# Optimization experiments

Measured on AMD Instinct MI355X. Metric: run time of the kernel, lower is better.

Reference implementation:

```python
import jax, jax.numpy as jnp
import numpy as np

B, T, D, N, K, H = 2, 2048, 2048, 16, 8, 128
WIN = 1024                      # sliding_window_size
SOFT_CAP = 50.0                 # attn_logits_soft_cap
SCALAR = 0.08838834764831845    # query_pre_attn_scalar = head_dim**-0.5
K_MASK = -2.3819763e+38
ROPE_BASE = 10000.0
ROPE_SCALE = 1.0


def apply_rope(x, positions):
    # x: [B, T, heads, H]; positions: [B, T]
    head_dim = x.shape[-1]
    half = head_dim // 2
    timescale = ROPE_BASE ** (2.0 * jnp.arange(half, dtype=jnp.float32) / head_dim)
    sinusoid = positions[..., None].astype(jnp.float32) / timescale / ROPE_SCALE  # [B,T,half]
    sin = jnp.sin(sinusoid)[:, :, None, :]
    cos = jnp.cos(sinusoid)[:, :, None, :]
    first, second = jnp.split(x, 2, axis=-1)
    return jnp.concatenate(
        [first * cos - second * sin, second * cos + first * sin], axis=-1
    ).astype(x.dtype)


def setup_inputs() -> dict:
    key = jax.random.key(0)
    k0, k1, k2, k3 = jax.random.split(key, 4)
    x = jax.random.normal(k0, (B, T, D), jnp.float32)
    wq = jax.random.normal(k1, (N, D, H), jnp.float32) * (D ** -0.5)
    wkv = jax.random.normal(k2, (2, K, D, H), jnp.float32) * (D ** -0.5)
    wo = jax.random.normal(k3, (N, H, D), jnp.float32) * ((N * H) ** -0.5)
    segment_pos = jnp.broadcast_to(jnp.arange(T, dtype=jnp.int32), (B, T))
    attn_mask = jnp.broadcast_to(jnp.tril(jnp.ones((T, T), dtype=bool)), (B, T, T))  # causal
    return {"x": x, "wq": wq, "wkv": wkv, "wo": wo,
            "segment_pos": segment_pos, "attn_mask": attn_mask}


def reference(x, wq, wkv, wo, segment_pos, attn_mask):
    # --- projections ---
    q = jnp.einsum('BTD,NDH->BTNH', x, wq)          # [B,T,N,H]
    kv = jnp.einsum('BTD,CKDH->CBTKH', x, wkv)      # [2,B,T,K,H]
    k_proj, v_proj = kv[0], kv[1]
    # --- RoPE + query scaling ---
    q = apply_rope(q, segment_pos) * SCALAR
    k_proj = apply_rope(k_proj, segment_pos)
    # --- GQA logits ---
    G = N // K
    qg = q.reshape(B, T, K, G, H)
    logits = jnp.einsum('BTKGH,BSKH->BTKGS', qg, k_proj).reshape(B, T, N, T)
    # --- soft cap ---
    logits = jnp.tanh(logits / SOFT_CAP) * SOFT_CAP
    # --- sliding-window mask combined with causal attn_mask ---
    all_ones = jnp.ones(attn_mask.shape, dtype=attn_mask.dtype)
    sliding_mask = jnp.triu(all_ones, -WIN + 1) * jnp.tril(all_ones, WIN - 1)
    mask = sliding_mask * attn_mask                  # [B,T,S]
    padded_logits = jnp.where(mask[:, :, None, :], logits, K_MASK)
    probs = jax.nn.softmax(padded_logits, axis=-1).astype(k_proj.dtype)
    # --- GQA weighted values ---
    encoded = jnp.einsum('BTKGS,BSKH->BTKGH',
                         probs.reshape(B, T, K, G, T), v_proj).reshape(B, T, N, H)
    # --- output projection ---
    return jnp.einsum('BTNH,NHD->BTD', encoded, wo)
```

## Files before the change

### kernel.cpp

```cpp
#include <hip/hip_runtime.h>
#include <stdint.h>

#define BDIM 2
#define TDIM 2048
#define DDIM 2048
#define NHEADS 16
#define KVH 8
#define HDIM 128
#define WINSZ 1024
#define BT (BDIM*TDIM)
#define NHD (NHEADS*HDIM)
#define QKVC 4096

typedef unsigned short u16;
typedef __attribute__((ext_vector_type(8))) short bf16x8;
typedef __attribute__((ext_vector_type(4))) float f32x4;

__device__ __forceinline__ u16 f2bf(float f) {
  union { float f; unsigned u; } v; v.f = f;
  unsigned r = v.u + 0x7FFFu + ((v.u >> 16) & 1u);
  return (u16)(r >> 16);
}
__device__ __forceinline__ float bf2f(u16 u) {
  union { unsigned u; float f; } v; v.u = ((unsigned)u) << 16;
  return v.f;
}

__device__ __forceinline__ void gl_lds16(const u16* g, u16* l) {
  __builtin_amdgcn_global_load_lds((const __attribute__((address_space(1))) void*)g,
                                   (__attribute__((address_space(3))) void*)l, 16, 0, 0);
}

__global__ __launch_bounds__(256) void k_prep(const float* __restrict__ x, const float* __restrict__ wq,
                                              const float* __restrict__ wkv, const float* __restrict__ wo,
                                              const int* __restrict__ seg,
                                              u16* __restrict__ x_bf, u16* __restrict__ wt_qkv,
                                              u16* __restrict__ wo_t, float2* __restrict__ tab) {
  const int id = blockIdx.x, tid = threadIdx.x;
  if (id < 8192) {
    __shared__ float tl0[32][33];
    int tx = tid & 31, ty = tid >> 5;
    int r0 = (id & 127) * 32, c0 = (id >> 7) * 32;
    #pragma unroll
    for (int i = 0; i < 4; i++) {
      int r = r0 + tx, c = c0 + ty + i*8;
      const float* sp; size_t off;
      if (r < 2048) { sp = wq; off = (size_t)(r >> 7)*262144u + (size_t)(r & 127); }
      else { int j = r - 2048; sp = wkv; off = (size_t)((j >> 10)*8 + ((j >> 7) & 7))*262144u + (size_t)(j & 127); }
      off += (size_t)c * 128u;
      tl0[tx][ty + i*8] = sp[off];
    }
    __syncthreads();
    #pragma unroll
    for (int i = 0; i < 4; i++) {
      int rl = ty + i*8;
      wt_qkv[(size_t)(r0 + rl)*2048u + (size_t)(c0 + tx)] = f2bf(tl0[rl][tx]);
    }
  } else if (id < 16384) {
    int i = (id - 8192)*256 + tid;
    float4 v = ((const float4*)x)[i];
    ushort4 o;
    o.x = f2bf(v.x); o.y = f2bf(v.y); o.z = f2bf(v.z); o.w = f2bf(v.w);
    ((ushort4*)x_bf)[i] = o;
  } else if (id < 20480) {
    __shared__ float tl1[32][33];
    int id3 = id - 16384;
    int tx = tid & 31, ty = tid >> 5;
    int r0 = (id3 & 63) * 32, c0 = (id3 >> 6) * 32;
    #pragma unroll
    for (int i = 0; i < 4; i++) {
      int r = r0 + tx, c = c0 + ty + i*8;
      tl1[tx][ty + i*8] = wo[(size_t)c * 2048u + (size_t)r];
    }
    __syncthreads();
    #pragma unroll
    for (int i = 0; i < 4; i++) {
      int rl = ty + i*8;
      wo_t[(size_t)(r0 + rl)*2048u + (size_t)(c0 + tx)] = f2bf(tl1[rl][tx]);
    }
  } else {
    int bt = (id - 20480)*4 + (tid >> 6);
    int i = tid & 63;
    int pos = seg[bt];
    float inv_ts = exp2f(-(float)i * (13.287712379549449f/64.0f));
    float ang = (float)pos * inv_ts;
    tab[(size_t)bt*64 + i] = make_float2(cosf(ang), sinf(ang));
  }
}

template<int F32OUT>
__global__ __launch_bounds__(256) void k_gemm(const u16* __restrict__ A, const u16* __restrict__ Bt,
                                              void* __restrict__ Cout, int M, int Ncols, int Kdim, int ldc) {
  __shared__ u16 As[128*64];
  __shared__ u16 Bs[128*64];
  const int tid = threadIdx.x, lane = tid & 63, wave = tid >> 6;
  const int bid = blockIdx.x;
  const int xcd = bid & 7, idx = bid >> 3;
  const int m0 = (((xcd & 3) << 3) + (idx & 7)) * 128;
  const int n0 = (((xcd >> 2) << 3) + (idx >> 3)) * 128;
  const int wr = wave >> 1, wc = wave & 1;
  const int l15 = lane & 15, lg = lane >> 4;
  f32x4 acc[4][4] = {};
  for (int kt = 0; kt < Kdim; kt += 64) {
    __syncthreads();
    #pragma unroll
    for (int i = 0; i < 4; i++) {
      int chb = i*256 + wave*64;
      int ch = chb + lane;
      int r = ch >> 3, cc = ch & 7;
      gl_lds16(A + (size_t)(m0 + r)*Kdim + kt + cc*8, As + chb*8);
      gl_lds16(Bt + (size_t)(n0 + r)*Kdim + kt + cc*8, Bs + chb*8);
    }
    __syncthreads();
    #pragma unroll
    for (int ks = 0; ks < 2; ks++) {
      bf16x8 af[4], bf[4];
      int kk = ks*32 + lg*8;
      #pragma unroll
      for (int mt = 0; mt < 4; mt++) af[mt] = *(const bf16x8*)(As + (wr*64 + mt*16 + l15)*64 + kk);
      #pragma unroll
      for (int nt = 0; nt < 4; nt++) bf[nt] = *(const bf16x8*)(Bs + (wc*64 + nt*16 + l15)*64 + kk);
      #pragma unroll
      for (int mt = 0; mt < 4; mt++)
        #pragma unroll
        for (int nt = 0; nt < 4; nt++)
          acc[mt][nt] = __builtin_amdgcn_mfma_f32_16x16x32_bf16(af[mt], bf[nt], acc[mt][nt], 0, 0, 0);
    }
  }
  #pragma unroll
  for (int mt = 0; mt < 4; mt++) {
    int row = m0 + wr*64 + mt*16 + lg*4;
    #pragma unroll
    for (int nt = 0; nt < 4; nt++) {
      int col = n0 + wc*64 + nt*16 + l15;
      #pragma unroll
      for (int j = 0; j < 4; j++) {
        if (F32OUT) ((float*)Cout)[(size_t)(row + j)*ldc + col] = acc[mt][nt][j];
        else        ((u16*)Cout)[(size_t)(row + j)*ldc + col] = f2bf(acc[mt][nt][j]);
      }
    }
  }
}

template<int F32OUT>
__global__ __launch_bounds__(512, 2) void k_gemm8(const u16* __restrict__ A, const u16* __restrict__ Bt,
                                                  void* __restrict__ Cout, int M, int Ncols, int Kdim, int ldc) {
  __shared__ u16 As[2][256*64];
  __shared__ u16 Bs[2][256*64];
  const int tid = threadIdx.x, lane = tid & 63, wave = tid >> 6;
  const int l15 = lane & 15, lg = lane >> 4;
  const int wm = wave >> 2, wn = wave & 3;
  const int gx = M >> 8, gy = Ncols >> 8;
  const int nwg = gx * gy;
  int bid = blockIdx.x;
  int q = nwg >> 3, r = nwg & 7;
  int xcd = bid & 7, idx = bid >> 3;
  int wg = (xcd < r ? xcd*(q+1) : r*(q+1) + (xcd - r)*q) + idx;
  const int m0 = (wg % gx) * 256, n0 = (wg / gx) * 256;

  const int st_r = tid >> 3;
  const int st_c = (tid & 7) ^ (st_r & 7);

  const u16* Ag = A + (size_t)(m0 + st_r)*Kdim + st_c*8;
  const u16* Bg = Bt + (size_t)(n0 + st_r)*Kdim + st_c*8;

  auto stage = [&](int t, int h) {
    int buf = t & 1;
    if (h < 2) {
      const u16* g = Bg + (size_t)(h*128)*Kdim + t*64;
      u16* d = &Bs[buf][h*8192 + wave*512];
      gl_lds16(g, d);
      gl_lds16(g + (size_t)64*Kdim, d + 4096);
    } else {
      int hh = h - 2;
      const u16* g = Ag + (size_t)(hh*128)*Kdim + t*64;
      u16* d = &As[buf][hh*8192 + wave*512];
      gl_lds16(g, d);
      gl_lds16(g + (size_t)64*Kdim, d + 4096);
    }
  };

  const int aBase = (wm*128 + l15) * 128;
  const int bBase = (wn*64 + l15) * 128;
  const int kx0 = ((lg) ^ (l15 & 7)) << 4;
  const int kx1 = ((4 + lg) ^ (l15 & 7)) << 4;

  f32x4 acc[8][4] = {};
  bf16x8 af[4][2], bfr[4][2];

  stage(0,0); stage(0,1); stage(0,2); stage(0,3);
  asm volatile("s_waitcnt vmcnt(4)" ::: "memory");
  stage(1,0); stage(1,1); stage(1,2);
  asm volatile("s_waitcnt vmcnt(6)" ::: "memory");
  __builtin_amdgcn_s_barrier();

  const int NT = Kdim >> 6;

#define MFMA_Q(MS, NS)                                                          \
  { _Pragma("unroll") for (int mf = 0; mf < 4; mf++)                            \
    _Pragma("unroll") for (int nf = 0; nf < 2; nf++) {                          \
      acc[(MS)+mf][(NS)+nf] = __builtin_amdgcn_mfma_f32_16x16x32_bf16(af[mf][0], bfr[(NS)+nf][0], acc[(MS)+mf][(NS)+nf], 0, 0, 0); \
      acc[(MS)+mf][(NS)+nf] = __builtin_amdgcn_mfma_f32_16x16x32_bf16(af[mf][1], bfr[(NS)+nf][1], acc[(MS)+mf][(NS)+nf], 0, 0, 0); \
  } }

  for (int t = 0; t < NT; ++t) {
    const int cur = t & 1;
    const char* Ab = (const char*)&As[cur][0];
    const char* Bb = (const char*)&Bs[cur][0];
    #pragma unroll
    for (int mf = 0; mf < 4; mf++) {
      af[mf][0] = *(const bf16x8*)(Ab + aBase + mf*2048 + kx0);
      af[mf][1] = *(const bf16x8*)(Ab + aBase + mf*2048 + kx1);
    }
    #pragma unroll
    for (int nf = 0; nf < 2; nf++) {
      bfr[nf][0] = *(const bf16x8*)(Bb + bBase + nf*2048 + kx0);
      bfr[nf][1] = *(const bf16x8*)(Bb + bBase + nf*2048 + kx1);
    }
    if (t + 1 < NT) stage(t+1, 3);
    asm volatile("s_waitcnt lgkmcnt(8)" ::: "memory");
    __builtin_amdgcn_s_barrier();
    asm volatile("" ::: "memory");
    __builtin_amdgcn_s_setprio(1);
    MFMA_Q(0, 0)
    __builtin_amdgcn_s_setprio(0);
    __builtin_amdgcn_s_barrier();
    #pragma unroll
    for (int nf = 2; nf < 4; nf++) {
      bfr[nf][0] = *(const bf16x8*)(Bb + bBase + nf*2048 + kx0);
      bfr[nf][1] = *(const bf16x8*)(Bb + bBase + nf*2048 + kx1);
    }
    __builtin_amdgcn_s_barrier();
    asm volatile("" ::: "memory");
    __builtin_amdgcn_s_setprio(1);
    MFMA_Q(0, 2)
    __builtin_amdgcn_s_setprio(0);
    __builtin_amdgcn_s_barrier();
    #pragma unroll
    for (int mf = 0; mf < 4; mf++) {
      af[mf][0] = *(const bf16x8*)(Ab + aBase + 8192 + mf*2048 + kx0);
      af[mf][1] = *(const bf16x8*)(Ab + aBase + 8192 + mf*2048 + kx1);
    }
    if (t + 2 < NT) { stage(t+2, 0); stage(t+2, 1); }
    __builtin_amdgcn_s_barrier();
    asm volatile("" ::: "memory");
    __builtin_amdgcn_s_setprio(1);
    MFMA_Q(4, 2)
    __builtin_amdgcn_s_setprio(0);
    __builtin_amdgcn_s_barrier();
    if (t + 2 < NT) {
      stage(t+2, 2);
      asm volatile("s_waitcnt vmcnt(6)" ::: "memory");
    } else if (t + 1 < NT) {
      asm volatile("s_waitcnt vmcnt(0)" ::: "memory");
    }
    __builtin_amdgcn_s_barrier();
    asm volatile("" ::: "memory");
    __builtin_amdgcn_s_setprio(1);
    MFMA_Q(4, 0)
    __builtin_amdgcn_s_setprio(0);
    __builtin_amdgcn_s_barrier();
  }
#undef MFMA_Q

  #pragma unroll
  for (int mf = 0; mf < 8; mf++) {
    int row = m0 + wm*128 + mf*16 + lg*4;
    #pragma unroll
    for (int nf = 0; nf < 4; nf++) {
      int col = n0 + wn*64 + nf*16 + l15;
      #pragma unroll
      for (int j = 0; j < 4; j++) {
        if (F32OUT) ((float*)Cout)[(size_t)(row + j)*ldc + col] = acc[mf][nf][j];
        else        ((u16*)Cout)[(size_t)(row + j)*ldc + col] = f2bf(acc[mf][nf][j]);
      }
    }
  }
}

__global__ __launch_bounds__(256) void k_kvt(u16* __restrict__ qkv, const float2* __restrict__ tab,
                                             u16* __restrict__ vT) {
  const int id = blockIdx.x, tid = threadIdx.x;
  if (id < 4096) {
    const int bt = id;
    const int kh = tid >> 5, ii = (tid & 31) * 2;
    u16* row = qkv + (size_t)bt*QKVC + 2048 + kh*128 + ii;
    const float2 c0 = tab[(size_t)bt*64 + ii];
    const float2 c1 = tab[(size_t)bt*64 + ii + 1];
    unsigned fu = *(const unsigned*)row;
    unsigned su = *(const unsigned*)(row + 64);
    float f0 = bf2f((u16)(fu & 0xffff)), f1 = bf2f((u16)(fu >> 16));
    float s0 = bf2f((u16)(su & 0xffff)), s1 = bf2f((u16)(su >> 16));
    unsigned ro = (unsigned)f2bf(f0*c0.x - s0*c0.y) | ((unsigned)f2bf(f1*c1.x - s1*c1.y) << 16);
    unsigned rs = (unsigned)f2bf(s0*c0.x + f0*c0.y) | ((unsigned)f2bf(s1*c1.x + f1*c1.y) << 16);
    *(unsigned*)row = ro;
    *(unsigned*)(row + 64) = rs;
  } else {
    __shared__ u16 tl[32][33];
    const int id2 = id - 4096;
    const int tx = tid & 31, ty = tid >> 5;
    const int t0 = (id2 & 63)*32, h0 = ((id2 >> 6) & 3)*32, bk = id2 >> 8;
    const u16* src = qkv + (size_t)(bk >> 3)*TDIM*QKVC + 3072 + (bk & 7)*HDIM;
    #pragma unroll
    for (int i = 0; i < 4; i++)
      tl[ty + i*8][tx] = src[(size_t)(t0 + ty + i*8)*QKVC + h0 + tx];
    __syncthreads();
    u16* dst = vT + (size_t)bk*HDIM*TDIM;
    #pragma unroll
    for (int i = 0; i < 4; i++)
      dst[(size_t)(h0 + ty + i*8)*TDIM + t0 + tx] = tl[tx][ty + i*8];
  }
}

__device__ __forceinline__ void stage_tiles(const u16* __restrict__ kg, const u16* __restrict__ vg,
                                            u16* ldsK, u16* ldsV, int tid) {
  const int w = tid >> 6;
  const int rK = tid >> 4, cK = tid & 15;
  u16* dK = ldsK + w*512;
  gl_lds16(kg + (size_t)rK*QKVC + ((cK ^ (rK & 15)) << 3), dK);
  gl_lds16(kg + (size_t)(rK + 32)*QKVC + ((cK ^ ((rK + 32) & 15)) << 3), dK + 4096);
  const int rV = tid >> 3, cV = tid & 7;
  u16* dV = ldsV + w*512;
  gl_lds16(vg + (size_t)rV*TDIM + ((cV ^ (rV & 7)) << 3), dV);
  gl_lds16(vg + (size_t)(rV + 64)*TDIM + ((cV ^ ((rV + 64) & 7)) << 3), dV + 4096);
}

__global__ __launch_bounds__(512, 4) void k_attn(const u16* __restrict__ qkv, const u16* __restrict__ vT,
                                                 const float2* __restrict__ tab, u16* __restrict__ enc) {
  __shared__ u16 Kb[2][64*128];
  __shared__ u16 Vb[2][128*64];
  __shared__ u16 Pl[8][16*64];
  const int tid = threadIdx.x;
  const int lane = tid & 63, wave = tid >> 6;
  const int l15 = lane & 15, lg = lane >> 4;
  const int wg = blockIdx.x;
  const int lin = (wg & 7)*64 + (wg >> 3);
  const int qt = lin & 31, kvh = (lin >> 5) & 7, b = lin >> 8;
  const int n = kvh*2 + (wave >> 2);
  const int t0 = qt * 64;
  const int lo_row = t0 + (wave & 3)*16, hi_row = lo_row + 15;

  bf16x8 qf[4];
  {
    const int qrow = b*TDIM + lo_row + l15;
    const u16* qb = qkv + (size_t)qrow*QKVC + n*HDIM + lg*8;
    #pragma unroll
    for (int ks = 0; ks < 4; ks++) qf[ks] = *(const bf16x8*)(qb + ks*32);
    const float2* trow = tab + (size_t)qrow*64 + lg*8;
    const float SC = 0.08838834764831845f;
    #pragma unroll
    for (int ks = 0; ks < 2; ks++)
      #pragma unroll
      for (int e = 0; e < 8; e++) {
        float2 cs = trow[ks*32 + e];
        float f = bf2f((u16)qf[ks][e]), s = bf2f((u16)qf[ks+2][e]);
        qf[ks][e]   = (short)f2bf((f*cs.x - s*cs.y) * SC);
        qf[ks+2][e] = (short)f2bf((s*cs.x + f*cs.y) * SC);
      }
  }
  f32x4 o[8] = {};
  f32x4 o_l = {};
  const short one_bf = (short)0x3F80;
  const bf16x8 ones = {one_bf, one_bf, one_bf, one_bf, one_bf, one_bf, one_bf, one_bf};

  const u16* kgb = qkv + (size_t)(b*TDIM)*QKVC + 2048 + kvh*HDIM;
  const u16* vgb = vT + (size_t)(b*KVH + kvh)*HDIM*TDIM;

  const float L0 = 1.4426950408889634f;
  const float L1 = -1.9235933878519513e-4f;
  const float L2 = 3.0777094205631089e-8f;
  const float BIAS = -72.13475204444817f;

  const int s_begin = (t0 >= 1024) ? (t0 - 1024) : 0;
  stage_tiles(kgb + (size_t)s_begin*QKVC, vgb + s_begin, Kb[0], Vb[0], tid);
  int cur = 0;
  for (int s0 = s_begin; s0 <= t0; s0 += 64) {
    if (s0 + 64 <= t0) {
      stage_tiles(kgb + (size_t)(s0 + 64)*QKVC, vgb + (s0 + 64), Kb[cur ^ 1], Vb[cur ^ 1], tid);
      asm volatile("s_waitcnt vmcnt(4)" ::: "memory");
    } else {
      asm volatile("s_waitcnt vmcnt(0)" ::: "memory");
    }
    __builtin_amdgcn_s_barrier();
    __builtin_amdgcn_sched_barrier(0);

    const u16* Kc = Kb[cur];
    const u16* Vc = Vb[cur];
    f32x4 sc4[4];
    #pragma unroll
    for (int c = 0; c < 4; c++) {
      const int cLo = s0 + c*16;
      bool anyLive = (cLo <= hi_row) && (cLo + 15 >= lo_row - (WINSZ - 1));
      bool full    = (cLo + 15 <= lo_row) && (cLo >= hi_row - (WINSZ - 1));
      f32x4 a = {0.f, 0.f, 0.f, 0.f};
      if (anyLive) {
        int krow = c*16 + l15;
        __builtin_amdgcn_s_setprio(1);
        #pragma unroll
        for (int ks = 0; ks < 4; ks++) {
          bf16x8 kf = *(const bf16x8*)(Kc + krow*128 + (((ks*4 + lg) ^ l15) << 3));
          a = __builtin_amdgcn_mfma_f32_16x16x32_bf16(qf[ks], kf, a, 0, 0, 0);
        }
        __builtin_amdgcn_s_setprio(0);
        if (full) {
          #pragma unroll
          for (int j = 0; j < 4; j++) {
            float z = a[j];
            float u = z*z;
            float tt = __builtin_fmaf(u, __builtin_fmaf(u, L2, L1), L0);
            a[j] = exp2f(__builtin_fmaf(z, tt, BIAS));
          }
        } else {
          #pragma unroll
          for (int j = 0; j < 4; j++) {
            int scol = cLo + l15;
            int trow2 = lo_row + lg*4 + j;
            float z = a[j];
            float u = z*z;
            float tt = __builtin_fmaf(u, __builtin_fmaf(u, L2, L1), L0);
            float p = exp2f(__builtin_fmaf(z, tt, BIAS));
            bool ok = (scol <= trow2) && (scol >= trow2 - (WINSZ - 1));
            a[j] = ok ? p : 0.f;
          }
        }
      }
      sc4[c] = a;
    }
    #pragma unroll
    for (int c = 0; c < 4; c++)
      #pragma unroll
      for (int j = 0; j < 4; j++) {
        int prow = lg*4 + j, pcol = c*16 + l15;
        int off = prow*128 + pcol*2; off ^= (prow & 7) << 4;
        *(u16*)((char*)(&Pl[wave][0]) + off) = f2bf(sc4[c][j]);
      }
    __builtin_amdgcn_s_setprio(1);
    #pragma unroll
    for (int ks = 0; ks < 2; ks++) {
      int roff = l15*128 + ks*64 + lg*16; roff ^= (l15 & 7) << 4;
      bf16x8 pf = *(const bf16x8*)((char*)(&Pl[wave][0]) + roff);
      o_l = __builtin_amdgcn_mfma_f32_16x16x32_bf16(pf, ones, o_l, 0, 0, 0);
      #pragma unroll
      for (int ct = 0; ct < 8; ct++) {
        int vrow = ct*16 + l15;
        bf16x8 vf = *(const bf16x8*)(Vc + vrow*64 + (((ks*4 + lg) ^ (l15 & 7)) << 3));
        o[ct] = __builtin_amdgcn_mfma_f32_16x16x32_bf16(pf, vf, o[ct], 0, 0, 0);
      }
    }
    __builtin_amdgcn_s_setprio(0);
    __builtin_amdgcn_s_barrier();
    cur ^= 1;
  }
  #pragma unroll
  for (int j = 0; j < 4; j++) {
    float inv = __fdividef(1.f, o_l[j]);
    int row = lo_row + lg*4 + j;
    u16* eb = enc + (size_t)(b*TDIM + row)*NHD + n*HDIM;
    #pragma unroll
    for (int ct = 0; ct < 8; ct++)
      eb[ct*16 + l15] = f2bf(o[ct][j] * inv);
  }
}

extern "C" void kernel_launch(void* const* d_in, const int* in_sizes, int n_in,
                              void* d_out, int out_size, void* d_ws, size_t ws_size,
                              hipStream_t stream) {
  const float* x   = (const float*)d_in[0];
  const float* wq  = (const float*)d_in[1];
  const float* wkv = (const float*)d_in[2];
  const float* wo  = (const float*)d_in[3];
  const int*   seg = (const int*)d_in[4];
  float* out = (float*)d_out;

  char* ws = (char*)d_ws;
  u16*    x_bf   = (u16*)(ws);
  u16*    wt_qkv = (u16*)(ws + (16u << 20));
  u16*    qkv    = (u16*)(ws + (32u << 20));
  u16*    vT     = (u16*)(ws + (64u << 20));
  u16*    enc    = (u16*)(ws + (72u << 20));
  u16*    wo_t   = (u16*)(ws + (88u << 20));
  float2* tab    = (float2*)(ws + (96u << 20));

  k_prep<<<dim3(21504), 256, 0, stream>>>(x, wq, wkv, wo, seg, x_bf, wt_qkv, wo_t, tab);
  k_gemm8<0><<<dim3((BT/256)*(QKVC/256)), 512, 0, stream>>>(x_bf, wt_qkv, qkv, BT, QKVC, DDIM, QKVC);
  k_kvt<<<dim3(8192), 256, 0, stream>>>(qkv, tab, vT);
  k_attn<<<dim3(512), 512, 0, stream>>>(qkv, vT, tab, enc);
  k_gemm<1><<<dim3(512), 256, 0, stream>>>(enc, wo_t, out, BT, DDIM, NHD, DDIM);
}
```

Baseline: 207.0 us.

## Fuse RoPE and query scaling into QKV GEMM epilogue

Each wave in the QKV GEMM now owns column pairs 64 apart within a head, instead of a contiguous 64-column slab. This lets the epilogue apply RoPE to Q and K, plus the query scale, in registers before the bf16 store. The separate K-RoPE pass in the old kvt kernel is dropped, leaving a V-transpose-only kernel, and the per-block Q RoPE in the attention kernel is removed. The aim is to avoid extra global read/write passes over K and the redundant Q RoPE work in attention. The trade-offs are a strided B-fragment LDS read pattern, a table load in the GEMM epilogue, and bf16 conversion switched to the library intrinsic.

```diff
diff --git a/kernel.cpp b/kernel.cpp
--- a/kernel.cpp
+++ b/kernel.cpp
@@ -1,4 +1,5 @@
 #include <hip/hip_runtime.h>
+#include <hip/hip_bf16.h>
 #include <stdint.h>
 
 #define BDIM 2
@@ -24,6 +25,10 @@
 __device__ __forceinline__ float bf2f(u16 u) {
   union { unsigned u; float f; } v; v.u = ((unsigned)u) << 16;
   return v.f;
+}
+__device__ __forceinline__ u16 cvt_bf(float f) {
+  __hip_bfloat16 hb = __float2bfloat16(f);
+  return *reinterpret_cast<u16*>(&hb);
 }
 
 __device__ __forceinline__ void gl_lds16(const u16* g, u16* l) {
@@ -142,9 +147,9 @@
   }
 }
 
-template<int F32OUT>
 __global__ __launch_bounds__(512, 2) void k_gemm8(const u16* __restrict__ A, const u16* __restrict__ Bt,
-                                                  void* __restrict__ Cout, int M, int Ncols, int Kdim, int ldc) {
+                                                  u16* __restrict__ Cout, const float2* __restrict__ tab,
+                                                  int M, int Ncols, int Kdim, int ldc) {
   __shared__ u16 As[2][256*64];
   __shared__ u16 Bs[2][256*64];
   const int tid = threadIdx.x, lane = tid & 63, wave = tid >> 6;
@@ -181,7 +186,7 @@
   };
 
   const int aBase = (wm*128 + l15) * 128;
-  const int bBase = (wn*64 + l15) * 128;
+  const int bBase = (wn*16 + l15) * 128;
   const int kx0 = ((lg) ^ (l15 & 7)) << 4;
   const int kx1 = ((4 + lg) ^ (l15 & 7)) << 4;
 
@@ -214,8 +219,8 @@
     }
     #pragma unroll
     for (int nf = 0; nf < 2; nf++) {
-      bfr[nf][0] = *(const bf16x8*)(Bb + bBase + nf*2048 + kx0);
-      bfr[nf][1] = *(const bf16x8*)(Bb + bBase + nf*2048 + kx1);
+      bfr[nf][0] = *(const bf16x8*)(Bb + bBase + nf*8192 + kx0);
+      bfr[nf][1] = *(const bf16x8*)(Bb + bBase + nf*8192 + kx1);
     }
     if (t + 1 < NT) stage(t+1, 3);
     asm volatile("s_waitcnt lgkmcnt(8)" ::: "memory");
@@ -227,8 +232,8 @@
     __builtin_amdgcn_s_barrier();
     #pragma unroll
     for (int nf = 2; nf < 4; nf++) {
-      bfr[nf][0] = *(const bf16x8*)(Bb + bBase + nf*2048 + kx0);
-      bfr[nf][1] = *(const bf16x8*)(Bb + bBase + nf*2048 + kx1);
+      bfr[nf][0] = *(const bf16x8*)(Bb + bBase + nf*8192 + kx0);
+      bfr[nf][1] = *(const bf16x8*)(Bb + bBase + nf*8192 + kx1);
     }
     __builtin_amdgcn_s_barrier();
     asm volatile("" ::: "memory");
@@ -263,53 +268,52 @@
   }
 #undef MFMA_Q
 
+  const int type = (n0 < 2048) ? 0 : (n0 < 3072 ? 1 : 2);
+  const float SC = 0.08838834764831845f;
   #pragma unroll
   for (int mf = 0; mf < 8; mf++) {
     int row = m0 + wm*128 + mf*16 + lg*4;
-    #pragma unroll
-    for (int nf = 0; nf < 4; nf++) {
-      int col = n0 + wn*64 + nf*16 + l15;
+    if (type < 2) {
       #pragma unroll
       for (int j = 0; j < 4; j++) {
-        if (F32OUT) ((float*)Cout)[(size_t)(row + j)*ldc + col] = acc[mf][nf][j];
-        else        ((u16*)Cout)[(size_t)(row + j)*ldc + col] = f2bf(acc[mf][nf][j]);
-      }
-    }
-  }
-}
-
-__global__ __launch_bounds__(256) void k_kvt(u16* __restrict__ qkv, const float2* __restrict__ tab,
-                                             u16* __restrict__ vT) {
+        float2 cs = tab[(size_t)(row + j)*64 + wn*16 + l15];
+        #pragma unroll
+        for (int pp = 0; pp < 4; pp += 2) {
+          float f = acc[mf][pp][j], s = acc[mf][pp+1][j];
+          float oa = f*cs.x - s*cs.y;
+          float ob = s*cs.x + f*cs.y;
+          if (type == 0) { oa *= SC; ob *= SC; }
+          int col = n0 + pp*64 + wn*16 + l15;
+          Cout[(size_t)(row + j)*ldc + col]      = cvt_bf(oa);
+          Cout[(size_t)(row + j)*ldc + col + 64] = cvt_bf(ob);
+        }
+      }
+    } else {
+      #pragma unroll
+      for (int nf = 0; nf < 4; nf++) {
+        int col = n0 + nf*64 + wn*16 + l15;
+        #pragma unroll
+        for (int j = 0; j < 4; j++)
+          Cout[(size_t)(row + j)*ldc + col] = f2bf(acc[mf][nf][j]);
+      }
+    }
+  }
+}
+
+__global__ __launch_bounds__(256) void k_vt(const u16* __restrict__ qkv, u16* __restrict__ vT) {
+  __shared__ u16 tl[32][33];
   const int id = blockIdx.x, tid = threadIdx.x;
-  if (id < 4096) {
-    const int bt = id;
-    const int kh = tid >> 5, ii = (tid & 31) * 2;
-    u16* row = qkv + (size_t)bt*QKVC + 2048 + kh*128 + ii;
-    const float2 c0 = tab[(size_t)bt*64 + ii];
-    const float2 c1 = tab[(size_t)bt*64 + ii + 1];
-    unsigned fu = *(const unsigned*)row;
-    unsigned su = *(const unsigned*)(row + 64);
-    float f0 = bf2f((u16)(fu & 0xffff)), f1 = bf2f((u16)(fu >> 16));
-    float s0 = bf2f((u16)(su & 0xffff)), s1 = bf2f((u16)(su >> 16));
-    unsigned ro = (unsigned)f2bf(f0*c0.x - s0*c0.y) | ((unsigned)f2bf(f1*c1.x - s1*c1.y) << 16);
-    unsigned rs = (unsigned)f2bf(s0*c0.x + f0*c0.y) | ((unsigned)f2bf(s1*c1.x + f1*c1.y) << 16);
-    *(unsigned*)row = ro;
-    *(unsigned*)(row + 64) = rs;
-  } else {
-    __shared__ u16 tl[32][33];
-    const int id2 = id - 4096;
-    const int tx = tid & 31, ty = tid >> 5;
-    const int t0 = (id2 & 63)*32, h0 = ((id2 >> 6) & 3)*32, bk = id2 >> 8;
-    const u16* src = qkv + (size_t)(bk >> 3)*TDIM*QKVC + 3072 + (bk & 7)*HDIM;
-    #pragma unroll
-    for (int i = 0; i < 4; i++)
-      tl[ty + i*8][tx] = src[(size_t)(t0 + ty + i*8)*QKVC + h0 + tx];
-    __syncthreads();
-    u16* dst = vT + (size_t)bk*HDIM*TDIM;
-    #pragma unroll
-    for (int i = 0; i < 4; i++)
-      dst[(size_t)(h0 + ty + i*8)*TDIM + t0 + tx] = tl[tx][ty + i*8];
-  }
+  const int tx = tid & 31, ty = tid >> 5;
+  const int t0 = (id & 63)*32, h0 = ((id >> 6) & 3)*32, bk = id >> 8;
+  const u16* src = qkv + (size_t)(bk >> 3)*TDIM*QKVC + 3072 + (bk & 7)*HDIM;
+  #pragma unroll
+  for (int i = 0; i < 4; i++)
+    tl[ty + i*8][tx] = src[(size_t)(t0 + ty + i*8)*QKVC + h0 + tx];
+  __syncthreads();
+  u16* dst = vT + (size_t)bk*HDIM*TDIM;
+  #pragma unroll
+  for (int i = 0; i < 4; i++)
+    dst[(size_t)(h0 + ty + i*8)*TDIM + t0 + tx] = tl[tx][ty + i*8];
 }
 
 __device__ __forceinline__ void stage_tiles(const u16* __restrict__ kg, const u16* __restrict__ vg,
@@ -326,7 +330,7 @@
 }
 
 __global__ __launch_bounds__(512, 4) void k_attn(const u16* __restrict__ qkv, const u16* __restrict__ vT,
-                                                 const float2* __restrict__ tab, u16* __restrict__ enc) {
+                                                 u16* __restrict__ enc) {
   __shared__ u16 Kb[2][64*128];
   __shared__ u16 Vb[2][128*64];
   __shared__ u16 Pl[8][16*64];
@@ -342,21 +346,9 @@
 
   bf16x8 qf[4];
   {
-    const int qrow = b*TDIM + lo_row + l15;
-    const u16* qb = qkv + (size_t)qrow*QKVC + n*HDIM + lg*8;
+    const u16* qb = qkv + (size_t)(b*TDIM + lo_row + l15)*QKVC + n*HDIM + lg*8;
     #pragma unroll
     for (int ks = 0; ks < 4; ks++) qf[ks] = *(const bf16x8*)(qb + ks*32);
-    const float2* trow = tab + (size_t)qrow*64 + lg*8;
-    const float SC = 0.08838834764831845f;
-    #pragma unroll
-    for (int ks = 0; ks < 2; ks++)
-      #pragma unroll
-      for (int e = 0; e < 8; e++) {
-        float2 cs = trow[ks*32 + e];
-        float f = bf2f((u16)qf[ks][e]), s = bf2f((u16)qf[ks+2][e]);
-        qf[ks][e]   = (short)f2bf((f*cs.x - s*cs.y) * SC);
-        qf[ks+2][e] = (short)f2bf((s*cs.x + f*cs.y) * SC);
-      }
   }
   f32x4 o[8] = {};
   f32x4 o_l = {};
@@ -432,7 +424,7 @@
       for (int j = 0; j < 4; j++) {
         int prow = lg*4 + j, pcol = c*16 + l15;
         int off = prow*128 + pcol*2; off ^= (prow & 7) << 4;
-        *(u16*)((char*)(&Pl[wave][0]) + off) = f2bf(sc4[c][j]);
+        *(u16*)((char*)(&Pl[wave][0]) + off) = cvt_bf(sc4[c][j]);
       }
     __builtin_amdgcn_s_setprio(1);
     #pragma unroll
@@ -458,7 +450,7 @@
     u16* eb = enc + (size_t)(b*TDIM + row)*NHD + n*HDIM;
     #pragma unroll
     for (int ct = 0; ct < 8; ct++)
-      eb[ct*16 + l15] = f2bf(o[ct][j] * inv);
+      eb[ct*16 + l15] = cvt_bf(o[ct][j] * inv);
   }
 }
 
@@ -482,8 +474,8 @@
   float2* tab    = (float2*)(ws + (96u << 20));
 
   k_prep<<<dim3(21504), 256, 0, stream>>>(x, wq, wkv, wo, seg, x_bf, wt_qkv, wo_t, tab);
-  k_gemm8<0><<<dim3((BT/256)*(QKVC/256)), 512, 0, stream>>>(x_bf, wt_qkv, qkv, BT, QKVC, DDIM, QKVC);
-  k_kvt<<<dim3(8192), 256, 0, stream>>>(qkv, tab, vT);
-  k_attn<<<dim3(512), 512, 0, stream>>>(qkv, vT, tab, enc);
+  k_gemm8<<<dim3((BT/256)*(QKVC/256)), 512, 0, stream>>>(x_bf, wt_qkv, qkv, tab, BT, QKVC, DDIM, QKVC);
+  k_vt<<<dim3(4096), 256, 0, stream>>>(qkv, vT);
+  k_attn<<<dim3(512), 512, 0, stream>>>(qkv, vT, enc);
   k_gemm<1><<<dim3(512), 256, 0, stream>>>(enc, wo_t, out, BT, DDIM, NHD, DDIM);
 }
```

After: 201.3 us. 2.8% less time.
